# Kernel tuning notes

Measured on AMD Instinct MI355X. Metric: run time of the kernel, lower is better.

## Reference

```python
import jax, jax.numpy as jnp
import numpy as np
from jax.scipy.special import logsumexp

N, M, D = 4096, 4096, 512
MASS = 0.9
REG = 0.1
REG_KL = 0.01
ITERS = 100


def setup_inputs() -> dict:
    key = jax.random.key(0)
    k0, k1 = jax.random.split(key)
    return {
        "ft0": jax.random.normal(k0, (N, D), dtype=jnp.float32),
        "ft1": jax.random.normal(k1, (M, D), dtype=jnp.float32),
        "bin_score": jnp.float32(0.4),
    }


def reference(ft0, ft1, bin_score):
    # all rows have norm >> 1e-8 for randn inputs -> foreground masks are all True
    f0 = ft0 / jnp.linalg.norm(ft0, axis=-1, keepdims=True)
    f1 = ft1 / jnp.linalg.norm(ft1, axis=-1, keepdims=True)
    cos_sim = f0 @ f1.T                       # [N, M]
    n, m = cos_sim.shape

    # partial OT marginals with dustbin mass (get_partial_distributions)
    a = jnp.concatenate([jnp.full((n,), MASS / n, jnp.float32),
                         jnp.array([1.0 - MASS], jnp.float32)])
    b = jnp.concatenate([jnp.full((m,), MASS / m, jnp.float32),
                         jnp.array([1.0 - MASS], jnp.float32)])
    log_mu, log_nu = jnp.log(a), jnp.log(b)   # [n+1], [m+1]

    # augment score matrix with dustbin row/col (get_partial_ot_problem)
    top = jnp.concatenate([cos_sim, jnp.broadcast_to(bin_score, (n, 1))], axis=1)
    bot = jnp.broadcast_to(bin_score, (1, m + 1))
    couplings = jnp.concatenate([top, bot], axis=0)   # [n+1, m+1]

    lmba = 1.0 / REG                         # = 10.0
    phi = REG_KL / (REG_KL + 1.0 / lmba)     # = 0.01 / 0.11
    Z = lmba * couplings

    def body(carry, _):
        u, v = carry
        u = (log_mu - logsumexp(Z + v[None, :] * lmba, axis=1)) / lmba * phi
        v = (log_nu - logsumexp(Z + u[:, None] * lmba, axis=0)) / lmba * phi
        return (u, v), None

    u0 = jnp.zeros((n + 1,), jnp.float32)
    v0 = jnp.zeros((m + 1,), jnp.float32)
    (u, v), _ = jax.lax.scan(body, (u0, v0), None, length=ITERS)

    prob = jnp.exp(Z + u[:, None] * lmba + v[None, :] * lmba)
    # prob_add_bkg with all-True masks: identity placement, zero the corner
    return prob.at[-1, -1].set(0.0)
```

## Files before the change

kernel.cpp:

```cpp
#include <hip/hip_runtime.h>
#include <math.h>

#define Nn 4096
#define Mm 4096
#define Dd 512
#define NP 4097
#define NPB 4104

#define PHI 0.09090909090909091f
#define LMU_IN  (-8.4231266823771690f)
#define LMU_BIN (-2.3025850929940457f)
#define LOG_NP  8.3180489582454150f

typedef __attribute__((ext_vector_type(8))) __bf16 bf16x8;
typedef __attribute__((ext_vector_type(4))) float  f32x4;

__device__ __forceinline__ void load_lds16(const __bf16* g, __bf16* l) {
    __builtin_amdgcn_global_load_lds(
        (__attribute__((address_space(1))) void*)g,
        (__attribute__((address_space(3))) void*)l,
        16, 0, 0);
}

__device__ __forceinline__ float block_allreduce_256(float v, float* sb) {
    #pragma unroll
    for (int off = 32; off > 0; off >>= 1) v += __shfl_down(v, off, 64);
    __syncthreads();
    if ((threadIdx.x & 63) == 0) sb[threadIdx.x >> 6] = v;
    __syncthreads();
    return sb[0] + sb[1] + sb[2] + sb[3];
}

__global__ __launch_bounds__(256) void normalize_bins_kernel(
    const float* __restrict__ F0, const float* __restrict__ F1,
    const float* __restrict__ binp,
    __bf16* __restrict__ A, __bf16* __restrict__ B, _Float16* __restrict__ Ef,
    float* __restrict__ S0, float* __restrict__ TcA) {
    __shared__ float sb[4];
    const int row = blockIdx.x;
    const float* src = (row < Nn) ? (F0 + (size_t)row * Dd)
                                  : (F1 + (size_t)(row - Nn) * Dd);
    __bf16* dst = (row < Nn) ? (A + (size_t)row * Dd)
                             : (B + (size_t)(row - Nn) * Dd);
    const float2 x = ((const float2*)src)[threadIdx.x];
    const float s = block_allreduce_256(x.x * x.x + x.y * x.y, sb);
    const float rn = rsqrtf(s);
    dst[2 * threadIdx.x]     = (__bf16)(x.x * rn);
    dst[2 * threadIdx.x + 1] = (__bf16)(x.y * rn);

    if (row < 17) {
        const int j = row * 256 + threadIdx.x;
        if (j < NP) Ef[(size_t)Nn * NPB + j] = (_Float16)__expf(10.0f * binp[0]);
    } else if (row < 33) {
        const int i = (row - 17) * 256 + threadIdx.x;
        Ef[(size_t)i * NPB + Mm] = (_Float16)__expf(10.0f * binp[0]);
    } else if (row < 50) {
        const int k = (row - 33) * 256 + threadIdx.x;
        if (k < NP) S0[k] = 0.f;
    } else if (row < 67) {
        const int k = (row - 50) * 256 + threadIdx.x;
        if (k < NP) TcA[k] = 0.f;
    }
}

#define BKh 32
__global__ __launch_bounds__(512, 2) void gemm_rowsum_kernel(
    const __bf16* __restrict__ A, const __bf16* __restrict__ B,
    _Float16* __restrict__ Ef, float* __restrict__ S0) {
    __shared__ __align__(16) __bf16 As[2][2][256 * BKh];
    __shared__ __align__(16) __bf16 Bs[2][2][256 * BKh];
    const int tid = threadIdx.x;
    const int l = tid & 63, wv = tid >> 6;
    const int wm = wv >> 2, wn = wv & 3;
    const int ln = l & 15, lq = l >> 4;

    const int bid = blockIdx.x;
    const int xcd = bid & 7, sub = bid >> 3;
    const int by = (xcd & 3) * 4 + (sub >> 3);
    const int bx = (xcd >> 2) * 8 + (sub & 7);
    const int row0 = by << 8, col0 = bx << 8;

    f32x4 acc[8][4];
    #pragma unroll
    for (int i = 0; i < 8; ++i)
        #pragma unroll
        for (int j = 0; j < 4; ++j) acc[i][j] = (f32x4){0.f, 0.f, 0.f, 0.f};

    size_t aG[2], bG[2]; int qE[2];
    #pragma unroll
    for (int p = 0; p < 2; ++p) {
        const int q = tid + p * 512;
        const int r = q >> 2, c = q & 3;
        const int cg = c ^ ((r >> 1) & 3);
        aG[p] = (size_t)(row0 + r) * Dd + cg * 8;
        bG[p] = (size_t)(col0 + r) * Dd + cg * 8;
        qE[p] = q * 8;
    }

    auto STAGE_UNIT = [&](int nb, int tt, int u) {
        const size_t kofs = (size_t)(tt * 64 + (u >> 1) * 32);
        if ((u & 1) == 0) {
            load_lds16(A + aG[0] + kofs, &As[nb][u >> 1][qE[0]]);
            load_lds16(A + aG[1] + kofs, &As[nb][u >> 1][qE[1]]);
        } else {
            load_lds16(B + bG[0] + kofs, &Bs[nb][u >> 1][qE[0]]);
            load_lds16(B + bG[1] + kofs, &Bs[nb][u >> 1][qE[1]]);
        }
    };

    #define WAITV(N) asm volatile("s_waitcnt vmcnt(" #N ")" ::: "memory")
    #define BAR() __builtin_amdgcn_s_barrier()

    const int swz2 = (ln >> 1) & 3;

    STAGE_UNIT(0, 0, 0); STAGE_UNIT(0, 0, 1);
    STAGE_UNIT(0, 0, 2); STAGE_UNIT(0, 0, 3);
    WAITV(4); BAR();

    #pragma unroll
    for (int t = 0; t < 8; ++t) {
        const int buf = t & 1, nbuf = buf ^ 1;
        #pragma unroll
        for (int ks = 0; ks < 2; ++ks) {
            bf16x8 bfr[4];
            #pragma unroll
            for (int half = 0; half < 2; ++half) {
                const int p = ks * 2 + half;
                if (half == 0) {
                    #pragma unroll
                    for (int ni = 0; ni < 4; ++ni) {
                        const int r = wn * 64 + ni * 16 + ln;
                        bfr[ni] = *(const bf16x8*)
                            &Bs[buf][ks][r * BKh + ((lq ^ swz2) * 8)];
                    }
                }
                bf16x8 af[4];
                #pragma unroll
                for (int i = 0; i < 4; ++i) {
                    const int r = wm * 128 + half * 64 + i * 16 + ln;
                    af[i] = *(const bf16x8*)
                        &As[buf][ks][r * BKh + ((lq ^ swz2) * 8)];
                }
                if (t < 7) STAGE_UNIT(nbuf, t + 1, p);
                if (t < 7 || p == 0) { WAITV(4); }
                else if (p == 1)     { WAITV(0); }
                BAR();
                __builtin_amdgcn_s_setprio(1);
                #pragma unroll
                for (int i = 0; i < 4; ++i)
                    #pragma unroll
                    for (int ni = 0; ni < 4; ++ni)
                        acc[half * 4 + i][ni] =
                            __builtin_amdgcn_mfma_f32_16x16x32_bf16(
                                af[i], bfr[ni], acc[half * 4 + i][ni], 0, 0, 0);
                __builtin_amdgcn_s_setprio(0);
                BAR();
            }
        }
    }
    #undef WAITV
    #undef BAR

    #pragma unroll
    for (int mi = 0; mi < 8; ++mi) {
        #pragma unroll
        for (int r = 0; r < 4; ++r) {
            const int gi = row0 + wm * 128 + mi * 16 + lq * 4 + r;
            _Float16* bRow = Ef + (size_t)gi * NPB + col0 + wn * 64 + ln;
            float rs = 0.f;
            #pragma unroll
            for (int ni = 0; ni < 4; ++ni) {
                const float e = __expf(10.0f * acc[mi][ni][r]);
                bRow[ni * 16] = (_Float16)e;
                rs += e;
            }
            rs += __shfl_down(rs, 8, 64);
            rs += __shfl_down(rs, 4, 64);
            rs += __shfl_down(rs, 2, 64);
            rs += __shfl_down(rs, 1, 64);
            if (ln == 0) atomicAdd(&S0[gi], rs);
        }
    }
}

__global__ __launch_bounds__(256) void wvec_kernel(
    const float* __restrict__ Tc, float* __restrict__ W,
    float* __restrict__ Zero) {
    const int j = blockIdx.x * 256 + threadIdx.x;
    if (j < NP) {
        const float lnu = (j < Mm) ? LMU_IN : LMU_BIN;
        W[j] = __expf(PHI * (lnu - __logf(Tc[j])));
        if (Zero) Zero[j] = 0.f;
    }
}

__global__ __launch_bounds__(256) void col_pass_kernel(
    const _Float16* __restrict__ Ef, const float* __restrict__ S0,
    const float* __restrict__ eUarr, const float* __restrict__ binp,
    float* __restrict__ Tc, const int mode) {
    __shared__ float evl[128];
    const int tid = threadIdx.x;
    const int t = blockIdx.x;
    const int sI = blockIdx.y;
    const int r0 = sI * 128;

    if (tid < 128) {
        const int r = r0 + tid;
        float ev;
        if (mode == 0) {
            const float ebin = __expf(10.0f * binp[0]);
            ev = __expf(PHI * (LMU_IN - __logf(S0[r] + ebin)));
        } else {
            ev = eUarr[r];
        }
        evl[tid] = ev;
    }
    __syncthreads();

    const int j0 = t * 512 + tid * 2;
    const unsigned short* base = (const unsigned short*)Ef;
    float s0 = 0.f, s1 = 0.f;
    #pragma unroll 16
    for (int k = 0; k < 128; ++k) {
        const int r = r0 + k;
        union { unsigned u; _Float16 h[2]; } e;
        e.u = *(const unsigned*)(base + (size_t)r * NPB + j0);
        const float ev = evl[k];
        s0 += (float)e.h[0] * ev;
        s1 += (float)e.h[1] * ev;
    }

    float ev4096 = 0.f;
    if (sI == 31) {
        ev4096 = (mode == 0)
               ? __expf(PHI * (LMU_BIN - (LOG_NP + 10.0f * binp[0])))
               : eUarr[Nn];
        union { unsigned u; _Float16 h[2]; } e;
        e.u = *(const unsigned*)(base + (size_t)Nn * NPB + j0);
        s0 += (float)e.h[0] * ev4096;
        s1 += (float)e.h[1] * ev4096;
    }
    atomicAdd(&Tc[j0], s0);
    atomicAdd(&Tc[j0 + 1], s1);

    if (t == 0 && tid < 128) {
        float sc = (float)Ef[(size_t)(r0 + tid) * NPB + Mm] * evl[tid];
        if (sI == 31 && tid == 0)
            sc += (float)Ef[(size_t)Nn * NPB + Mm] * ev4096;
        #pragma unroll
        for (int off = 32; off > 0; off >>= 1) sc += __shfl_down(sc, off, 64);
        if ((tid & 63) == 0) atomicAdd(&Tc[Mm], sc);
    }
}

__global__ __launch_bounds__(256) void row_pass2_kernel(
    const _Float16* __restrict__ Ef, const float* __restrict__ W1,
    float* __restrict__ eU) {
    __shared__ float sb[4];
    __shared__ float wl[NP];
    const int tid = threadIdx.x;

    for (int c = tid; c < 1024; c += 256)
        ((float4*)wl)[c] = ((const float4*)W1)[c];
    if (tid == 0) wl[Mm] = W1[Mm];
    __syncthreads();

    const int i0 = blockIdx.x * 8;
    #pragma unroll 1
    for (int k = 0; k < 8; ++k) {
        const int i = i0 + k;
        if (i >= NP) break;
        const uint4* rowp = (const uint4*)(Ef + (size_t)i * NPB);
        float s = 0.f;
        #pragma unroll
        for (int c = 0; c < 2; ++c) {
            const int chunk = c * 256 + tid;
            union { uint4 u; _Float16 h[8]; } e;
            e.u = rowp[chunk];
            const float4 w0 = *(const float4*)&wl[chunk * 8];
            const float4 w1 = *(const float4*)&wl[chunk * 8 + 4];
            s += (float)e.h[0] * w0.x + (float)e.h[1] * w0.y
               + (float)e.h[2] * w0.z + (float)e.h[3] * w0.w
               + (float)e.h[4] * w1.x + (float)e.h[5] * w1.y
               + (float)e.h[6] * w1.z + (float)e.h[7] * w1.w;
        }
        if (tid == 0) s += (float)Ef[(size_t)i * NPB + Mm] * wl[Mm];
        s = block_allreduce_256(s, sb);
        if (tid == 0) {
            const float lmu = (i < Nn) ? LMU_IN : LMU_BIN;
            eU[i] = __expf(PHI * (lmu - __logf(s)));
        }
    }
}

__global__ __launch_bounds__(256) void finish_kernel(
    const _Float16* __restrict__ Ef, const float* __restrict__ eU,
    const float* __restrict__ W2, float* __restrict__ out) {
    __shared__ float wl[NP];
    const int tid = threadIdx.x;
    for (int c = tid; c < 1024; c += 256)
        ((float4*)wl)[c] = ((const float4*)W2)[c];
    if (tid == 0) wl[Mm] = W2[Mm];
    __syncthreads();

    const int i0 = blockIdx.x * 8;
    #pragma unroll 1
    for (int k = 0; k < 8; ++k) {
        const int i = i0 + k;
        if (i >= NP) break;
        const float sU = eU[i];
        const unsigned short* erow = (const unsigned short*)(Ef + (size_t)i * NPB);
        float* orow = out + (size_t)i * NP;
        #pragma unroll
        for (int c = 0; c < 16; ++c) {
            const int j = c * 256 + tid;
            union { unsigned short u; _Float16 h; } e;
            e.u = erow[j];
            orow[j] = (float)e.h * sU * wl[j];
        }
        if (tid == 0) {
            float v = (float)Ef[(size_t)i * NPB + Mm] * sU * wl[Mm];
            if (i == Nn) v = 0.f;
            orow[Mm] = v;
        }
    }
}


extern "C" void kernel_launch(void* const* d_in, const int* in_sizes, int n_in,
                              void* d_out, int out_size, void* d_ws, size_t ws_size,
                              hipStream_t stream) {
    const float* ft0 = (const float*)d_in[0];
    const float* ft1 = (const float*)d_in[1];
    const float* bin = (const float*)d_in[2];
    float* out = (float*)d_out;

    const size_t ABF_B = (size_t)Nn * Dd * 2;
    const size_t EBF_B = (size_t)NP * NPB * 2;
    const size_t VEC_B = 16400;
    __bf16*   Abf = (__bf16*)d_ws;
    __bf16*   Bbf = (__bf16*)((char*)d_ws + ABF_B);
    _Float16* Ef  = (_Float16*)((char*)d_ws + 2 * ABF_B);
    float*    eU  = (float*)((char*)d_ws + 2 * ABF_B + EBF_B);
    float*    S0  = (float*)((char*)d_ws + 2 * ABF_B + EBF_B + VEC_B);
    float*    TcA = (float*)((char*)d_ws + 2 * ABF_B + EBF_B + 2 * VEC_B);
    float*    TcB = (float*)((char*)d_ws + 2 * ABF_B + EBF_B + 3 * VEC_B);
    float*    W1  = (float*)((char*)d_ws + 2 * ABF_B + EBF_B + 4 * VEC_B);
    float*    W2  = (float*)((char*)d_ws + 2 * ABF_B + EBF_B + 5 * VEC_B);

    normalize_bins_kernel<<<Nn + Mm, 256, 0, stream>>>(ft0, ft1, bin,
                                                       Abf, Bbf, Ef, S0, TcA);
    gemm_rowsum_kernel<<<256, 512, 0, stream>>>(Abf, Bbf, Ef, S0);
    col_pass_kernel<<<dim3(8, 32), 256, 0, stream>>>(Ef, S0, eU, bin, TcA, 0);
    wvec_kernel<<<17, 256, 0, stream>>>(TcA, W1, TcB);
    row_pass2_kernel<<<513, 256, 0, stream>>>(Ef, W1, eU);
    col_pass_kernel<<<dim3(8, 32), 256, 0, stream>>>(Ef, S0, eU, bin, TcB, 1);
    wvec_kernel<<<17, 256, 0, stream>>>(TcB, W2, nullptr);
    finish_kernel<<<513, 256, 0, stream>>>(Ef, eU, W2, out);
}
```

Before: 180.8 us.

## Stage GEMM epilogue through LDS and vectorize finish kernel output stores

The GEMM epilogue now writes the exp'd fp16 tile into shared memory (reusing the A/B staging buffers) and then emits coalesced 16-byte row stores to Ef, replacing scattered 2-byte stores. The finish kernel is restructured to process 4 rows per block over a flattened contiguous output range with float4 stores, with a separate block for the dustbin row. This targets poor store coalescing in both kernels. In exchange it adds extra LDS traffic and barriers, plus per-element index math in finish.

```diff
diff --git a/kernel.cpp b/kernel.cpp
--- a/kernel.cpp
+++ b/kernel.cpp
@@ -64,11 +64,13 @@
 }
 
 #define BKh 32
+#define CLD 264
 __global__ __launch_bounds__(512, 2) void gemm_rowsum_kernel(
     const __bf16* __restrict__ A, const __bf16* __restrict__ B,
     _Float16* __restrict__ Ef, float* __restrict__ S0) {
-    __shared__ __align__(16) __bf16 As[2][2][256 * BKh];
-    __shared__ __align__(16) __bf16 Bs[2][2][256 * BKh];
+    __shared__ __align__(16) __bf16 smem[2][2][2][256 * BKh];
+    #define AS(b, k) (&smem[0][b][k][0])
+    #define BS(b, k) (&smem[1][b][k][0])
     const int tid = threadIdx.x;
     const int l = tid & 63, wv = tid >> 6;
     const int wm = wv >> 2, wn = wv & 3;
@@ -100,11 +102,11 @@
     auto STAGE_UNIT = [&](int nb, int tt, int u) {
         const size_t kofs = (size_t)(tt * 64 + (u >> 1) * 32);
         if ((u & 1) == 0) {
-            load_lds16(A + aG[0] + kofs, &As[nb][u >> 1][qE[0]]);
-            load_lds16(A + aG[1] + kofs, &As[nb][u >> 1][qE[1]]);
+            load_lds16(A + aG[0] + kofs, AS(nb, u >> 1) + qE[0]);
+            load_lds16(A + aG[1] + kofs, AS(nb, u >> 1) + qE[1]);
         } else {
-            load_lds16(B + bG[0] + kofs, &Bs[nb][u >> 1][qE[0]]);
-            load_lds16(B + bG[1] + kofs, &Bs[nb][u >> 1][qE[1]]);
+            load_lds16(B + bG[0] + kofs, BS(nb, u >> 1) + qE[0]);
+            load_lds16(B + bG[1] + kofs, BS(nb, u >> 1) + qE[1]);
         }
     };
 
@@ -131,7 +133,7 @@
                     for (int ni = 0; ni < 4; ++ni) {
                         const int r = wn * 64 + ni * 16 + ln;
                         bfr[ni] = *(const bf16x8*)
-                            &Bs[buf][ks][r * BKh + ((lq ^ swz2) * 8)];
+                            &BS(buf, ks)[r * BKh + ((lq ^ swz2) * 8)];
                     }
                 }
                 bf16x8 af[4];
@@ -139,7 +141,7 @@
                 for (int i = 0; i < 4; ++i) {
                     const int r = wm * 128 + half * 64 + i * 16 + ln;
                     af[i] = *(const bf16x8*)
-                        &As[buf][ks][r * BKh + ((lq ^ swz2) * 8)];
+                        &AS(buf, ks)[r * BKh + ((lq ^ swz2) * 8)];
                 }
                 if (t < 7) STAGE_UNIT(nbuf, t + 1, p);
                 if (t < 7 || p == 0) { WAITV(4); }
@@ -161,26 +163,45 @@
     #undef WAITV
     #undef BAR
 
-    #pragma unroll
-    for (int mi = 0; mi < 8; ++mi) {
-        #pragma unroll
-        for (int r = 0; r < 4; ++r) {
-            const int gi = row0 + wm * 128 + mi * 16 + lq * 4 + r;
-            _Float16* bRow = Ef + (size_t)gi * NPB + col0 + wn * 64 + ln;
-            float rs = 0.f;
+    _Float16* Cs = (_Float16*)&smem[0][0][0][0];
+    #pragma unroll
+    for (int pass = 0; pass < 2; ++pass) {
+        __syncthreads();
+        #pragma unroll
+        for (int m3 = 0; m3 < 4; ++m3) {
+            const int mi = pass * 4 + m3;
             #pragma unroll
-            for (int ni = 0; ni < 4; ++ni) {
-                const float e = __expf(10.0f * acc[mi][ni][r]);
-                bRow[ni * 16] = (_Float16)e;
-                rs += e;
+            for (int r = 0; r < 4; ++r) {
+                const int lr = wm * 64 + m3 * 16 + lq * 4 + r;
+                float rs = 0.f;
+                #pragma unroll
+                for (int ni = 0; ni < 4; ++ni) {
+                    const float e = __expf(10.0f * acc[mi][ni][r]);
+                    Cs[lr * CLD + wn * 64 + ni * 16 + ln] = (_Float16)e;
+                    rs += e;
+                }
+                rs += __shfl_down(rs, 8, 64);
+                rs += __shfl_down(rs, 4, 64);
+                rs += __shfl_down(rs, 2, 64);
+                rs += __shfl_down(rs, 1, 64);
+                if (ln == 0) {
+                    const int gi = row0 + wm * 128 + mi * 16 + lq * 4 + r;
+                    atomicAdd(&S0[gi], rs);
+                }
             }
-            rs += __shfl_down(rs, 8, 64);
-            rs += __shfl_down(rs, 4, 64);
-            rs += __shfl_down(rs, 2, 64);
-            rs += __shfl_down(rs, 1, 64);
-            if (ln == 0) atomicAdd(&S0[gi], rs);
-        }
-    }
+        }
+        __syncthreads();
+        #pragma unroll
+        for (int p = 0; p < 8; ++p) {
+            const int q = tid + p * 512;
+            const int lr = q >> 5, ck = q & 31;
+            const int gi = row0 + (lr >> 6) * 128 + pass * 64 + (lr & 63);
+            const uint4 v = *(const uint4*)&Cs[lr * CLD + ck * 8];
+            *(uint4*)(Ef + (size_t)gi * NPB + col0 + ck * 8) = v;
+        }
+    }
+    #undef AS
+    #undef BS
 }
 
 __global__ __launch_bounds__(256) void wvec_kernel(
@@ -297,31 +318,45 @@
     const _Float16* __restrict__ Ef, const float* __restrict__ eU,
     const float* __restrict__ W2, float* __restrict__ out) {
     __shared__ float wl[NP];
+    __shared__ float el[4];
     const int tid = threadIdx.x;
     for (int c = tid; c < 1024; c += 256)
         ((float4*)wl)[c] = ((const float4*)W2)[c];
     if (tid == 0) wl[Mm] = W2[Mm];
-    __syncthreads();
-
-    const int i0 = blockIdx.x * 8;
-    #pragma unroll 1
-    for (int k = 0; k < 8; ++k) {
-        const int i = i0 + k;
-        if (i >= NP) break;
-        const float sU = eU[i];
-        const unsigned short* erow = (const unsigned short*)(Ef + (size_t)i * NPB);
-        float* orow = out + (size_t)i * NP;
-        #pragma unroll
-        for (int c = 0; c < 16; ++c) {
-            const int j = c * 256 + tid;
+    const int i0 = blockIdx.x * 4;
+    if (tid < 4 && i0 + tid < NP) el[tid] = eU[i0 + tid];
+    __syncthreads();
+
+    if (blockIdx.x < 1024) {
+        const unsigned short* ef = (const unsigned short*)Ef;
+        float* ob = out + (size_t)i0 * NP;
+        #pragma unroll 4
+        for (int c = 0; c < 17; ++c) {
+            const int q = c * 256 + tid;
+            if (q >= 4097) break;
+            const int lf = q * 4;
+            float4 v;
+            float* vp = (float*)&v;
+            #pragma unroll
+            for (int e = 0; e < 4; ++e) {
+                const int lfe = lf + e;
+                const int re = (lfe >= NP) + (lfe >= 2 * NP) + (lfe >= 3 * NP);
+                const int j = lfe - re * NP;
+                const int i = i0 + re;
+                union { unsigned short u; _Float16 h; } ev;
+                ev.u = ef[(size_t)i * NPB + j];
+                vp[e] = (float)ev.h * el[re] * wl[j];
+            }
+            *(float4*)(ob + lf) = v;
+        }
+    } else {
+        const float sU = el[0];
+        const unsigned short* erow = (const unsigned short*)(Ef + (size_t)Nn * NPB);
+        float* orow = out + (size_t)Nn * NP;
+        for (int j = tid; j < NP; j += 256) {
             union { unsigned short u; _Float16 h; } e;
             e.u = erow[j];
-            orow[j] = (float)e.h * sU * wl[j];
-        }
-        if (tid == 0) {
-            float v = (float)Ef[(size_t)i * NPB + Mm] * sU * wl[Mm];
-            if (i == Nn) v = 0.f;
-            orow[Mm] = v;
+            orow[j] = (j == Mm) ? 0.f : (float)e.h * sU * wl[j];
         }
     }
 }
@@ -356,5 +391,5 @@
     row_pass2_kernel<<<513, 256, 0, stream>>>(Ef, W1, eU);
     col_pass_kernel<<<dim3(8, 32), 256, 0, stream>>>(Ef, S0, eU, bin, TcB, 1);
     wvec_kernel<<<17, 256, 0, stream>>>(TcB, W2, nullptr);
-    finish_kernel<<<513, 256, 0, stream>>>(Ef, eU, W2, out);
-}
+    finish_kernel<<<1025, 256, 0, stream>>>(Ef, eU, W2, out);
+}
```

Measured after the change: 186.0 us. 2.9% more time.

## Shrink GEMM tiles to 128x128 with triple buffering, LDS-staged epilogue, wave-per-row row pass

Applied to the files above, without the earlier changes.

The GEMM moves from 256x256 tiles with 512 threads to 128x128 tiles with 256 threads and 1024 blocks. It uses a three-stage LDS ring with one barrier per K step. The exp'd fp16 results are staged through LDS so global stores become coalesced 16-byte row writes. Separately, row_pass2 drops the LDS copy of the weight vector and the block reduction, giving each wave one row with a shuffle reduction. Smaller tiles fill more CUs but cost more global traffic per FLOP.

```diff
diff --git a/kernel.cpp b/kernel.cpp
--- a/kernel.cpp
+++ b/kernel.cpp
@@ -63,122 +63,118 @@
     }
 }
 
-#define BKh 32
-__global__ __launch_bounds__(512, 2) void gemm_rowsum_kernel(
+#define BKq 32
+#define CLD2 132
+__global__ __launch_bounds__(256) void gemm_rowsum_kernel(
     const __bf16* __restrict__ A, const __bf16* __restrict__ B,
     _Float16* __restrict__ Ef, float* __restrict__ S0) {
-    __shared__ __align__(16) __bf16 As[2][2][256 * BKh];
-    __shared__ __align__(16) __bf16 Bs[2][2][256 * BKh];
+    __shared__ __align__(16) __bf16 As[3][128 * BKq];
+    __shared__ __align__(16) __bf16 Bs[3][128 * BKq];
     const int tid = threadIdx.x;
     const int l = tid & 63, wv = tid >> 6;
-    const int wm = wv >> 2, wn = wv & 3;
+    const int wm = wv >> 1, wn = wv & 1;
     const int ln = l & 15, lq = l >> 4;
 
     const int bid = blockIdx.x;
     const int xcd = bid & 7, sub = bid >> 3;
-    const int by = (xcd & 3) * 4 + (sub >> 3);
-    const int bx = (xcd >> 2) * 8 + (sub & 7);
-    const int row0 = by << 8, col0 = bx << 8;
-
-    f32x4 acc[8][4];
-    #pragma unroll
-    for (int i = 0; i < 8; ++i)
+    const int by = (xcd & 3) * 8 + (sub >> 4);
+    const int bx = (xcd >> 2) * 16 + (sub & 15);
+    const int row0 = by << 7, col0 = bx << 7;
+
+    f32x4 acc[4][4];
+    #pragma unroll
+    for (int i = 0; i < 4; ++i)
         #pragma unroll
         for (int j = 0; j < 4; ++j) acc[i][j] = (f32x4){0.f, 0.f, 0.f, 0.f};
 
-    size_t aG[2], bG[2]; int qE[2];
+    const __bf16* aS[2]; const __bf16* bS[2]; int qE[2];
     #pragma unroll
     for (int p = 0; p < 2; ++p) {
-        const int q = tid + p * 512;
+        const int q = tid + p * 256;
         const int r = q >> 2, c = q & 3;
         const int cg = c ^ ((r >> 1) & 3);
-        aG[p] = (size_t)(row0 + r) * Dd + cg * 8;
-        bG[p] = (size_t)(col0 + r) * Dd + cg * 8;
+        aS[p] = A + (size_t)(row0 + r) * Dd + cg * 8;
+        bS[p] = B + (size_t)(col0 + r) * Dd + cg * 8;
         qE[p] = q * 8;
     }
 
-    auto STAGE_UNIT = [&](int nb, int tt, int u) {
-        const size_t kofs = (size_t)(tt * 64 + (u >> 1) * 32);
-        if ((u & 1) == 0) {
-            load_lds16(A + aG[0] + kofs, &As[nb][u >> 1][qE[0]]);
-            load_lds16(A + aG[1] + kofs, &As[nb][u >> 1][qE[1]]);
-        } else {
-            load_lds16(B + bG[0] + kofs, &Bs[nb][u >> 1][qE[0]]);
-            load_lds16(B + bG[1] + kofs, &Bs[nb][u >> 1][qE[1]]);
-        }
+    auto STAGE = [&](int b, int k0) {
+        load_lds16(aS[0] + k0, &As[b][qE[0]]);
+        load_lds16(aS[1] + k0, &As[b][qE[1]]);
+        load_lds16(bS[0] + k0, &Bs[b][qE[0]]);
+        load_lds16(bS[1] + k0, &Bs[b][qE[1]]);
     };
 
     #define WAITV(N) asm volatile("s_waitcnt vmcnt(" #N ")" ::: "memory")
     #define BAR() __builtin_amdgcn_s_barrier()
 
-    const int swz2 = (ln >> 1) & 3;
-
-    STAGE_UNIT(0, 0, 0); STAGE_UNIT(0, 0, 1);
-    STAGE_UNIT(0, 0, 2); STAGE_UNIT(0, 0, 3);
+    const int sw = (ln >> 1) & 3;
+
+    STAGE(0, 0); STAGE(1, BKq);
     WAITV(4); BAR();
 
     #pragma unroll
-    for (int t = 0; t < 8; ++t) {
-        const int buf = t & 1, nbuf = buf ^ 1;
-        #pragma unroll
-        for (int ks = 0; ks < 2; ++ks) {
-            bf16x8 bfr[4];
+    for (int t = 0; t < 16; ++t) {
+        const int buf = t % 3;
+        if (t < 14) STAGE((t + 2) % 3, (t + 2) * BKq);
+        bf16x8 bfr[4], af[4];
+        #pragma unroll
+        for (int ni = 0; ni < 4; ++ni)
+            bfr[ni] = *(const bf16x8*)
+                &Bs[buf][(wn * 64 + ni * 16 + ln) * BKq + (lq ^ sw) * 8];
+        #pragma unroll
+        for (int mi = 0; mi < 4; ++mi)
+            af[mi] = *(const bf16x8*)
+                &As[buf][(wm * 64 + mi * 16 + ln) * BKq + (lq ^ sw) * 8];
+        __builtin_amdgcn_s_setprio(1);
+        #pragma unroll
+        for (int mi = 0; mi < 4; ++mi)
             #pragma unroll
-            for (int half = 0; half < 2; ++half) {
-                const int p = ks * 2 + half;
-                if (half == 0) {
-                    #pragma unroll
-                    for (int ni = 0; ni < 4; ++ni) {
-                        const int r = wn * 64 + ni * 16 + ln;
-                        bfr[ni] = *(const bf16x8*)
-                            &Bs[buf][ks][r * BKh + ((lq ^ swz2) * 8)];
-                    }
-                }
-                bf16x8 af[4];
-                #pragma unroll
-                for (int i = 0; i < 4; ++i) {
-                    const int r = wm * 128 + half * 64 + i * 16 + ln;
-                    af[i] = *(const bf16x8*)
-                        &As[buf][ks][r * BKh + ((lq ^ swz2) * 8)];
-                }
-                if (t < 7) STAGE_UNIT(nbuf, t + 1, p);
-                if (t < 7 || p == 0) { WAITV(4); }
-                else if (p == 1)     { WAITV(0); }
-                BAR();
-                __builtin_amdgcn_s_setprio(1);
-                #pragma unroll
-                for (int i = 0; i < 4; ++i)
-                    #pragma unroll
-                    for (int ni = 0; ni < 4; ++ni)
-                        acc[half * 4 + i][ni] =
-                            __builtin_amdgcn_mfma_f32_16x16x32_bf16(
-                                af[i], bfr[ni], acc[half * 4 + i][ni], 0, 0, 0);
-                __builtin_amdgcn_s_setprio(0);
-                BAR();
-            }
-        }
+            for (int ni = 0; ni < 4; ++ni)
+                acc[mi][ni] = __builtin_amdgcn_mfma_f32_16x16x32_bf16(
+                    af[mi], bfr[ni], acc[mi][ni], 0, 0, 0);
+        __builtin_amdgcn_s_setprio(0);
+        if (t < 14)      { WAITV(4); BAR(); }
+        else if (t == 14){ WAITV(0); BAR(); }
     }
     #undef WAITV
     #undef BAR
 
-    #pragma unroll
-    for (int mi = 0; mi < 8; ++mi) {
-        #pragma unroll
-        for (int r = 0; r < 4; ++r) {
-            const int gi = row0 + wm * 128 + mi * 16 + lq * 4 + r;
-            _Float16* bRow = Ef + (size_t)gi * NPB + col0 + wn * 64 + ln;
-            float rs = 0.f;
+    _Float16* Cs = (_Float16*)&As[0][0];
+    #pragma unroll
+    for (int p = 0; p < 2; ++p) {
+        __syncthreads();
+        #pragma unroll
+        for (int m1 = 0; m1 < 2; ++m1) {
+            const int mi = p * 2 + m1;
             #pragma unroll
-            for (int ni = 0; ni < 4; ++ni) {
-                const float e = __expf(10.0f * acc[mi][ni][r]);
-                bRow[ni * 16] = (_Float16)e;
-                rs += e;
+            for (int r = 0; r < 4; ++r) {
+                const int lr = wm * 32 + m1 * 16 + lq * 4 + r;
+                float rs = 0.f;
+                #pragma unroll
+                for (int ni = 0; ni < 4; ++ni) {
+                    const float e = __expf(10.0f * acc[mi][ni][r]);
+                    Cs[lr * CLD2 + wn * 64 + ni * 16 + ln] = (_Float16)e;
+                    rs += e;
+                }
+                rs += __shfl_down(rs, 8, 64);
+                rs += __shfl_down(rs, 4, 64);
+                rs += __shfl_down(rs, 2, 64);
+                rs += __shfl_down(rs, 1, 64);
+                if (ln == 0) {
+                    const int gi = row0 + wm * 64 + mi * 16 + lq * 4 + r;
+                    atomicAdd(&S0[gi], rs);
+                }
             }
-            rs += __shfl_down(rs, 8, 64);
-            rs += __shfl_down(rs, 4, 64);
-            rs += __shfl_down(rs, 2, 64);
-            rs += __shfl_down(rs, 1, 64);
-            if (ln == 0) atomicAdd(&S0[gi], rs);
+        }
+        __syncthreads();
+        #pragma unroll
+        for (int pp = 0; pp < 4; ++pp) {
+            const int q = tid + pp * 256;
+            const int lr = q >> 4, ck = q & 15;
+            const int gi = row0 + (lr >> 5) * 64 + p * 32 + (lr & 31);
+            *(uint4*)(Ef + (size_t)gi * NPB + col0 + ck * 8) =
+                *(const uint4*)&Cs[lr * CLD2 + ck * 8];
         }
     }
 }
@@ -256,39 +252,36 @@
 __global__ __launch_bounds__(256) void row_pass2_kernel(
     const _Float16* __restrict__ Ef, const float* __restrict__ W1,
     float* __restrict__ eU) {
-    __shared__ float sb[4];
-    __shared__ float wl[NP];
     const int tid = threadIdx.x;
-
-    for (int c = tid; c < 1024; c += 256)
-        ((float4*)wl)[c] = ((const float4*)W1)[c];
-    if (tid == 0) wl[Mm] = W1[Mm];
-    __syncthreads();
-
+    const int wv = tid >> 6, l = tid & 63;
     const int i0 = blockIdx.x * 8;
-    #pragma unroll 1
-    for (int k = 0; k < 8; ++k) {
-        const int i = i0 + k;
-        if (i >= NP) break;
-        const uint4* rowp = (const uint4*)(Ef + (size_t)i * NPB);
-        float s = 0.f;
-        #pragma unroll
-        for (int c = 0; c < 2; ++c) {
-            const int chunk = c * 256 + tid;
-            union { uint4 u; _Float16 h[8]; } e;
-            e.u = rowp[chunk];
-            const float4 w0 = *(const float4*)&wl[chunk * 8];
-            const float4 w1 = *(const float4*)&wl[chunk * 8 + 4];
-            s += (float)e.h[0] * w0.x + (float)e.h[1] * w0.y
-               + (float)e.h[2] * w0.z + (float)e.h[3] * w0.w
-               + (float)e.h[4] * w1.x + (float)e.h[5] * w1.y
-               + (float)e.h[6] * w1.z + (float)e.h[7] * w1.w;
-        }
-        if (tid == 0) s += (float)Ef[(size_t)i * NPB + Mm] * wl[Mm];
-        s = block_allreduce_256(s, sb);
-        if (tid == 0) {
-            const float lmu = (i < Nn) ? LMU_IN : LMU_BIN;
-            eU[i] = __expf(PHI * (lmu - __logf(s)));
+    const float4* w4 = (const float4*)W1;
+
+    #pragma unroll
+    for (int k = 0; k < 2; ++k) {
+        const int i = i0 + k * 4 + wv;
+        if (i < NP) {
+            const uint4* rowp = (const uint4*)(Ef + (size_t)i * NPB);
+            float s = 0.f;
+            #pragma unroll
+            for (int c = 0; c < 8; ++c) {
+                const int chunk = c * 64 + l;
+                union { uint4 u; _Float16 h[8]; } e;
+                e.u = rowp[chunk];
+                const float4 w0 = w4[chunk * 2];
+                const float4 w1 = w4[chunk * 2 + 1];
+                s += (float)e.h[0] * w0.x + (float)e.h[1] * w0.y
+                   + (float)e.h[2] * w0.z + (float)e.h[3] * w0.w
+                   + (float)e.h[4] * w1.x + (float)e.h[5] * w1.y
+                   + (float)e.h[6] * w1.z + (float)e.h[7] * w1.w;
+            }
+            if (l == 0) s += (float)Ef[(size_t)i * NPB + Mm] * W1[Mm];
+            #pragma unroll
+            for (int off = 32; off > 0; off >>= 1) s += __shfl_down(s, off, 64);
+            if (l == 0) {
+                const float lmu = (i < Nn) ? LMU_IN : LMU_BIN;
+                eU[i] = __expf(PHI * (lmu - __logf(s)));
+            }
         }
     }
 }
@@ -350,7 +343,7 @@
 
     normalize_bins_kernel<<<Nn + Mm, 256, 0, stream>>>(ft0, ft1, bin,
                                                        Abf, Bbf, Ef, S0, TcA);
-    gemm_rowsum_kernel<<<256, 512, 0, stream>>>(Abf, Bbf, Ef, S0);
+    gemm_rowsum_kernel<<<1024, 256, 0, stream>>>(Abf, Bbf, Ef, S0);
     col_pass_kernel<<<dim3(8, 32), 256, 0, stream>>>(Ef, S0, eU, bin, TcA, 0);
     wvec_kernel<<<17, 256, 0, stream>>>(TcA, W1, TcB);
     row_pass2_kernel<<<513, 256, 0, stream>>>(Ef, W1, eU);
```

Result: slower. 187.7 us (+3.8%).
